# Kernel optimization log

Measured on AMD Instinct MI355X. Metric: run time of the kernel, lower is better.

Reference implementation:

```python
import jax, jax.numpy as jnp
import numpy as np

HEAD_DIM = 64
SCALE = HEAD_DIM ** (-0.5)


def setup_inputs() -> dict:
    key = jax.random.key(0)
    kq, kk, kv = jax.random.split(key, 3)
    B, H, S, D = 2, 12, 2048, HEAD_DIM
    query = jax.random.normal(kq, (B, H, S, D), dtype=jnp.float32)
    k = jax.random.normal(kk, (B, H, S, D), dtype=jnp.float32)
    v = jax.random.normal(kv, (B, H, S, D), dtype=jnp.float32)
    mask = jnp.ones((1, 1, S, S), dtype=jnp.int32)
    return {"query": query, "key": k, "value": v, "mask": mask}


def reference(query, key, value, mask):
    # scores: [B, H, S, S]
    scores = jnp.einsum("bhqd,bhkd->bhqk", query, key) * SCALE
    scores = jnp.where(mask == 0, -jnp.inf, scores)
    probs = jax.nn.softmax(scores, axis=-1)
    # dropout = 0.0 -> identity
    out = jnp.einsum("bhqk,bhkd->bhqd", probs, value)
    return out
```

## Files before the change

kernel.cpp:

```cpp
#include <hip/hip_runtime.h>

#define SDIM 2048
#define DDIM 64
#define QT   64
#define KT   64
#define NT   (SDIM / KT)
#define SCL2  (0.125f * 1.4426950408889634f)

typedef __attribute__((ext_vector_type(8))) short          bf16x8;
typedef __attribute__((ext_vector_type(4))) short          bf16x4;
typedef __attribute__((ext_vector_type(8))) unsigned short ushort8;
typedef __attribute__((ext_vector_type(4))) unsigned short us4;
typedef __attribute__((ext_vector_type(4))) float          f32x4;

__device__ __forceinline__ unsigned short f2bf(float x) {
    unsigned int u = __float_as_uint(x);
    u += 0x7FFFu + ((u >> 16) & 1u);
    return (unsigned short)(u >> 16);
}

__device__ __forceinline__ f32x4 mfma16(bf16x4 a, bf16x4 b, f32x4 c) {
#if __has_builtin(__builtin_amdgcn_mfma_f32_16x16x16bf16_1k)
    return __builtin_amdgcn_mfma_f32_16x16x16bf16_1k(a, b, c, 0, 0, 0);
#else
    asm volatile("v_mfma_f32_16x16x16_bf16 %0, %1, %2, %0" : "+v"(c) : "v"(a), "v"(b));
    return c;
#endif
}

__device__ __forceinline__ void cp16(const void* g, void* l) {
    __builtin_amdgcn_global_load_lds(
        (__attribute__((address_space(1))) void*)(uintptr_t)g,
        (__attribute__((address_space(3))) void*)(unsigned int)(uintptr_t)l,
        16, 0, 0);
}

__global__ __launch_bounds__(256)
void prep_kv(const float* __restrict__ Kp, const float* __restrict__ Vp,
             unsigned short* __restrict__ wsK, unsigned short* __restrict__ wsV)
{
    __shared__ alignas(16) unsigned short vstage[KT * DDIM];
    const int tid = threadIdx.x;
    const int t   = blockIdx.x;
    const int bh  = blockIdx.y;
    const size_t tb   = ((size_t)bh * NT + t) * (KT * DDIM);
    const size_t gsrc = (size_t)bh * SDIM * DDIM + (size_t)t * KT * DDIM;

    const int key = tid >> 2;
    const int d0  = (tid & 3) << 4;
    const int sw  = (key & 7) << 3;

    {
        const float* src = Kp + gsrc + key * DDIM + d0;
        float4 a0 = ((const float4*)src)[0];
        float4 a1 = ((const float4*)src)[1];
        float4 a2 = ((const float4*)src)[2];
        float4 a3 = ((const float4*)src)[3];
        ushort8 w0, w1;
        w0[0]=f2bf(a0.x); w0[1]=f2bf(a0.y); w0[2]=f2bf(a0.z); w0[3]=f2bf(a0.w);
        w0[4]=f2bf(a1.x); w0[5]=f2bf(a1.y); w0[6]=f2bf(a1.z); w0[7]=f2bf(a1.w);
        w1[0]=f2bf(a2.x); w1[1]=f2bf(a2.y); w1[2]=f2bf(a2.z); w1[3]=f2bf(a2.w);
        w1[4]=f2bf(a3.x); w1[5]=f2bf(a3.y); w1[6]=f2bf(a3.z); w1[7]=f2bf(a3.w);
        *(ushort8*)&wsK[tb + key * 64 + ( d0      ^ sw)] = w0;
        *(ushort8*)&wsK[tb + key * 64 + ((d0 + 8) ^ sw)] = w1;
    }
    {
        const float* src = Vp + gsrc + key * DDIM + d0;
        float4 a0 = ((const float4*)src)[0];
        float4 a1 = ((const float4*)src)[1];
        float4 a2 = ((const float4*)src)[2];
        float4 a3 = ((const float4*)src)[3];
        ushort8 w0, w1;
        w0[0]=f2bf(a0.x); w0[1]=f2bf(a0.y); w0[2]=f2bf(a0.z); w0[3]=f2bf(a0.w);
        w0[4]=f2bf(a1.x); w0[5]=f2bf(a1.y); w0[6]=f2bf(a1.z); w0[7]=f2bf(a1.w);
        w1[0]=f2bf(a2.x); w1[1]=f2bf(a2.y); w1[2]=f2bf(a2.z); w1[3]=f2bf(a2.w);
        w1[4]=f2bf(a3.x); w1[5]=f2bf(a3.y); w1[6]=f2bf(a3.z); w1[7]=f2bf(a3.w);
        *(ushort8*)&vstage[key * 64 + ( d0      ^ sw)] = w0;
        *(ushort8*)&vstage[key * 64 + ((d0 + 8) ^ sw)] = w1;
    }
    __syncthreads();
    {
        const int d  = tid >> 2;
        const int k0 = (tid & 3) << 4;
        const int m  = ((d & 7) << 1) ^ ((d >> 3) & 1);
        const int region = ((k0 >> 2) ^ (m & 12));
        unsigned short vals[16];
        #pragma unroll
        for (int j = 0; j < 16; ++j) {
            const int k = k0 + j;
            vals[j] = vstage[k * 64 + (d ^ ((k & 7) << 3))];
        }
        #pragma unroll
        for (int j = 0; j < 4; ++j) {
            us4 o = { vals[4*j], vals[4*j+1], vals[4*j+2], vals[4*j+3] };
            *(us4*)&wsV[tb + d * 64 + ((region | (j ^ (m & 3))) << 2)] = o;
        }
    }
}

__global__ __launch_bounds__(512)
void attn64_main(const float* __restrict__ Qp,
                 const unsigned short* __restrict__ wsK,
                 const unsigned short* __restrict__ wsV,
                 float* __restrict__ Op)
{
    __shared__ alignas(16) unsigned short kbuf[4][4096];
    __shared__ alignas(16) unsigned short vbuf[4][4096];

    const int tid  = threadIdx.x;
    const int lane = tid & 63;
    const int w    = tid >> 6;
    const int qg   = w & 3;
    const int par  = w >> 2;
    const int lo4  = lane & 15;
    const int hi2  = lane >> 4;
    const int l7s  = (lo4 & 7) << 3;
    const int vm   = ((lo4 & 7) << 1) ^ ((lo4 >> 3) & 1);

    const int qt = blockIdx.x;
    const int bh = blockIdx.y;

    const unsigned short* Kt = wsK + (size_t)bh * (SDIM * DDIM);
    const unsigned short* Vt = wsV + (size_t)bh * (SDIM * DDIM);

    cp16(Kt + tid * 8,        &kbuf[0][tid * 8]);
    cp16(Vt + tid * 8,        &vbuf[0][tid * 8]);
    cp16(Kt + 4096 + tid * 8, &kbuf[1][tid * 8]);
    cp16(Vt + 4096 + tid * 8, &vbuf[1][tid * 8]);

    bf16x8 qf[2];
    {
        const float* Qb = Qp + (size_t)bh * SDIM * DDIM;
        const int qrow = qt * QT + qg * 16 + lo4;
        #pragma unroll
        for (int ks = 0; ks < 2; ++ks) {
            const float* src = Qb + (size_t)qrow * DDIM + ks * 32 + hi2 * 8;
            float4 a = ((const float4*)src)[0];
            float4 b = ((const float4*)src)[1];
            bf16x8 tq;
            tq[0] = (short)f2bf(a.x * SCL2); tq[1] = (short)f2bf(a.y * SCL2);
            tq[2] = (short)f2bf(a.z * SCL2); tq[3] = (short)f2bf(a.w * SCL2);
            tq[4] = (short)f2bf(b.x * SCL2); tq[5] = (short)f2bf(b.y * SCL2);
            tq[6] = (short)f2bf(b.z * SCL2); tq[7] = (short)f2bf(b.w * SCL2);
            qf[ks] = tq;
        }
    }

    int kidx[2], vidx[4];
    #pragma unroll
    for (int ks = 0; ks < 2; ++ks) kidx[ks] = lo4 * 64 + ((ks * 32 + hi2 * 8) ^ l7s);
    #pragma unroll
    for (int n = 0; n < 4; ++n)   vidx[n]  = lo4 * 64 + (((4 * n + hi2) ^ vm) << 2);

    const short ov = (lo4 == 0) ? (short)0x3F80 : (short)0;
    const bf16x4 af = { ov, ov, ov, ov };

    f32x4 oacc[4];
    f32x4 acc5 = f32x4{0.f, 0.f, 0.f, 0.f};
    #pragma unroll
    for (int n = 0; n < 4; ++n) oacc[n] = f32x4{0.f, 0.f, 0.f, 0.f};

    const unsigned short* kbR0 = &kbuf[par][0];
    const unsigned short* vbR0 = &vbuf[par][0];
    const unsigned short* kbR1 = &kbuf[2 + par][0];
    const unsigned short* vbR1 = &vbuf[2 + par][0];

    const unsigned short* gk = Kt + 2 * 4096 + tid * 8;
    const unsigned short* gv = Vt + 2 * 4096 + tid * 8;

    auto tilebody = [&](const unsigned short* kb, const unsigned short* vb) {
        f32x4 s[4];
        #pragma unroll
        for (int n = 0; n < 4; ++n) s[n] = f32x4{0.f, 0.f, 0.f, 0.f};
        __builtin_amdgcn_s_setprio(1);
        #pragma unroll
        for (int ks = 0; ks < 2; ++ks) {
            #pragma unroll
            for (int n = 0; n < 4; ++n) {
                bf16x8 kf = *(const bf16x8*)&kb[kidx[ks] + n * 1024];
                s[n] = __builtin_amdgcn_mfma_f32_16x16x32_bf16(kf, qf[ks], s[n], 0, 0, 0);
            }
        }
        __builtin_amdgcn_s_setprio(0);
        bf16x4 pkk[4];
        #pragma unroll
        for (int n = 0; n < 4; ++n) {
            const float p0 = exp2f(s[n][0]);
            const float p1 = exp2f(s[n][1]);
            const float p2 = exp2f(s[n][2]);
            const float p3 = exp2f(s[n][3]);
            unsigned int lo, hi;
            asm("v_cvt_pk_bf16_f32 %0, %1, %2" : "=v"(lo) : "v"(p0), "v"(p1));
            asm("v_cvt_pk_bf16_f32 %0, %1, %2" : "=v"(hi) : "v"(p2), "v"(p3));
            union { unsigned int u[2]; bf16x4 v; } r;
            r.u[0] = lo; r.u[1] = hi;
            pkk[n] = r.v;
        }
        __builtin_amdgcn_s_setprio(1);
        #pragma unroll
        for (int n = 0; n < 4; ++n) {
            acc5 = mfma16(af, pkk[n], acc5);
            #pragma unroll
            for (int db = 0; db < 4; ++db) {
                bf16x4 vf = *(const bf16x4*)&vb[vidx[n] + db * 1024];
                oacc[db] = mfma16(vf, pkk[n], oacc[db]);
            }
        }
        __builtin_amdgcn_s_setprio(0);
    };

    asm volatile("s_waitcnt vmcnt(0) lgkmcnt(0)" ::: "memory");
    __builtin_amdgcn_s_barrier();

    #pragma unroll 1
    for (int j = 0; j < 8; ++j) {
        cp16(gk,        &kbuf[2][tid * 8]);
        cp16(gv,        &vbuf[2][tid * 8]);
        cp16(gk + 4096, &kbuf[3][tid * 8]);
        cp16(gv + 4096, &vbuf[3][tid * 8]);
        tilebody(kbR0, vbR0);
        asm volatile("s_waitcnt vmcnt(0) lgkmcnt(0)" ::: "memory");
        __builtin_amdgcn_s_barrier();
        if (j < 7) {
            cp16(gk + 8192,  &kbuf[0][tid * 8]);
            cp16(gv + 8192,  &vbuf[0][tid * 8]);
            cp16(gk + 12288, &kbuf[1][tid * 8]);
            cp16(gv + 12288, &vbuf[1][tid * 8]);
        }
        tilebody(kbR1, vbR1);
        asm volatile("s_waitcnt vmcnt(0) lgkmcnt(0)" ::: "memory");
        __builtin_amdgcn_s_barrier();
        gk += 16384;
        gv += 16384;
    }

    __syncthreads();
    float* comb = (float*)&kbuf[0][0];
    const int cbase = (qg * 64 + lane) * 20;
    if (par) {
        *(f32x4*)&comb[cbase]      = oacc[0];
        *(f32x4*)&comb[cbase + 4]  = oacc[1];
        *(f32x4*)&comb[cbase + 8]  = oacc[2];
        *(f32x4*)&comb[cbase + 12] = oacc[3];
        *(f32x4*)&comb[cbase + 16] = acc5;
    }
    __syncthreads();
    if (!par) {
        oacc[0] += *(const f32x4*)&comb[cbase];
        oacc[1] += *(const f32x4*)&comb[cbase + 4];
        oacc[2] += *(const f32x4*)&comb[cbase + 8];
        oacc[3] += *(const f32x4*)&comb[cbase + 12];
        acc5    += *(const f32x4*)&comb[cbase + 16];

        const float lsum = __shfl(acc5[0], lo4);
        const float inv = 1.f / lsum;
        const int q = qt * QT + qg * 16 + lo4;
        float* dst = Op + (size_t)bh * SDIM * DDIM + (size_t)q * DDIM;
        #pragma unroll
        for (int db = 0; db < 4; ++db) {
            float4 o = { oacc[db][0] * inv, oacc[db][1] * inv,
                         oacc[db][2] * inv, oacc[db][3] * inv };
            *(float4*)&dst[16 * db + hi2 * 4] = o;
        }
    }
}

__global__ __launch_bounds__(256)
void attn64_fallback(const float* __restrict__ Qp, const float* __restrict__ Kp,
                     const float* __restrict__ Vp, float* __restrict__ Op)
{
    __shared__ alignas(16) unsigned short kls[KT * DDIM];
    __shared__ alignas(16) unsigned short vls[DDIM * KT];
    __shared__ alignas(16) unsigned short pls[4][16 * KT];

    const int tid  = threadIdx.x;
    const int lane = tid & 63;
    const int wave = tid >> 6;
    const int lo4  = lane & 15;
    const int hi2  = lane >> 4;
    const int qt = blockIdx.x;
    const int bh = blockIdx.y;

    const size_t base = (size_t)bh * SDIM * DDIM;
    const float* Qb = Qp + base;
    const float* Kb = Kp + base;
    const float* Vb = Vp + base;
    float*       Ob = Op + base;

    bf16x8 qf[2];
    {
        const int qrow = qt * QT + wave * 16 + lo4;
        #pragma unroll
        for (int ks = 0; ks < 2; ++ks) {
            const float* src = Qb + (size_t)qrow * DDIM + ks * 32 + hi2 * 8;
            float4 a = ((const float4*)src)[0];
            float4 b = ((const float4*)src)[1];
            bf16x8 tq;
            tq[0] = (short)f2bf(a.x * SCL2); tq[1] = (short)f2bf(a.y * SCL2);
            tq[2] = (short)f2bf(a.z * SCL2); tq[3] = (short)f2bf(a.w * SCL2);
            tq[4] = (short)f2bf(b.x * SCL2); tq[5] = (short)f2bf(b.y * SCL2);
            tq[6] = (short)f2bf(b.z * SCL2); tq[7] = (short)f2bf(b.w * SCL2);
            qf[ks] = tq;
        }
    }

    float mrow[4], lrow[4];
    f32x4 oacc[4];
    #pragma unroll
    for (int r = 0; r < 4; ++r) { mrow[r] = -1e30f; lrow[r] = 0.f; }
    #pragma unroll
    for (int n = 0; n < 4; ++n) oacc[n] = f32x4{0.f, 0.f, 0.f, 0.f};

    for (int t0 = 0; t0 < SDIM; t0 += KT) {
        __syncthreads();
        {
            const int key = tid >> 2;
            const int d0  = (tid & 3) << 4;
            const float* src = Kb + (size_t)(t0 + key) * DDIM + d0;
            float4 a0 = ((const float4*)src)[0];
            float4 a1 = ((const float4*)src)[1];
            float4 a2 = ((const float4*)src)[2];
            float4 a3 = ((const float4*)src)[3];
            ushort8 w0, w1;
            w0[0]=f2bf(a0.x); w0[1]=f2bf(a0.y); w0[2]=f2bf(a0.z); w0[3]=f2bf(a0.w);
            w0[4]=f2bf(a1.x); w0[5]=f2bf(a1.y); w0[6]=f2bf(a1.z); w0[7]=f2bf(a1.w);
            w1[0]=f2bf(a2.x); w1[1]=f2bf(a2.y); w1[2]=f2bf(a2.z); w1[3]=f2bf(a2.w);
            w1[4]=f2bf(a3.x); w1[5]=f2bf(a3.y); w1[6]=f2bf(a3.z); w1[7]=f2bf(a3.w);
            const int sw = (key & 7) << 3;
            *(ushort8*)&kls[key * 64 + ( d0      ^ sw)] = w0;
            *(ushort8*)&kls[key * 64 + ((d0 + 8) ^ sw)] = w1;
        }
        {
            const int key = lane;
            const int d0  = wave << 4;
            const float* src = Vb + (size_t)(t0 + key) * DDIM + d0;
            float4 b0 = ((const float4*)src)[0];
            float4 b1 = ((const float4*)src)[1];
            float4 b2 = ((const float4*)src)[2];
            float4 b3 = ((const float4*)src)[3];
            float vv[16] = { b0.x,b0.y,b0.z,b0.w, b1.x,b1.y,b1.z,b1.w,
                             b2.x,b2.y,b2.z,b2.w, b3.x,b3.y,b3.z,b3.w };
            #pragma unroll
            for (int j = 0; j < 16; ++j) {
                const int d = d0 + j;
                vls[d * 64 + (key ^ ((d & 7) << 3))] = f2bf(vv[j]);
            }
        }
        __syncthreads();

        f32x4 s[4];
        #pragma unroll
        for (int n = 0; n < 4; ++n) s[n] = f32x4{0.f, 0.f, 0.f, 0.f};
        #pragma unroll
        for (int ks = 0; ks < 2; ++ks) {
            const int kb = ks * 32 + hi2 * 8;
            #pragma unroll
            for (int n = 0; n < 4; ++n) {
                const int key = lo4 + 16 * n;
                bf16x8 b = *(const bf16x8*)&kls[key * 64 + (kb ^ ((key & 7) << 3))];
                s[n] = __builtin_amdgcn_mfma_f32_16x16x32_bf16(qf[ks], b, s[n], 0, 0, 0);
            }
        }
        #pragma unroll
        for (int r = 0; r < 4; ++r) {
            float tmax = fmaxf(fmaxf(s[0][r], s[1][r]), fmaxf(s[2][r], s[3][r]));
            tmax = fmaxf(tmax, __shfl_xor(tmax, 1));
            tmax = fmaxf(tmax, __shfl_xor(tmax, 2));
            tmax = fmaxf(tmax, __shfl_xor(tmax, 4));
            tmax = fmaxf(tmax, __shfl_xor(tmax, 8));
            const float mn   = fmaxf(mrow[r], tmax);
            const float corr = exp2f(mrow[r] - mn);
            mrow[r] = mn;
            float rs = 0.f;
            #pragma unroll
            for (int n = 0; n < 4; ++n) {
                const float p = exp2f(s[n][r] - mn);
                s[n][r] = p;
                rs += p;
            }
            rs += __shfl_xor(rs, 1);
            rs += __shfl_xor(rs, 2);
            rs += __shfl_xor(rs, 4);
            rs += __shfl_xor(rs, 8);
            lrow[r] = lrow[r] * corr + rs;
            #pragma unroll
            for (int n = 0; n < 4; ++n) oacc[n][r] *= corr;
        }
        #pragma unroll
        for (int r = 0; r < 4; ++r) {
            const int q  = hi2 * 4 + r;
            const int sw = (q & 7) << 3;
            #pragma unroll
            for (int n = 0; n < 4; ++n)
                pls[wave][q * 64 + ((lo4 + 16 * n) ^ sw)] = f2bf(s[n][r]);
        }
        __syncthreads();
        #pragma unroll
        for (int ks = 0; ks < 2; ++ks) {
            const int kb = ks * 32 + hi2 * 8;
            bf16x8 a = *(const bf16x8*)&pls[wave][lo4 * 64 + (kb ^ ((lo4 & 7) << 3))];
            #pragma unroll
            for (int n = 0; n < 4; ++n) {
                const int d = 16 * n + lo4;
                bf16x8 b = *(const bf16x8*)&vls[d * 64 + (kb ^ ((d & 7) << 3))];
                oacc[n] = __builtin_amdgcn_mfma_f32_16x16x32_bf16(a, b, oacc[n], 0, 0, 0);
            }
        }
    }
    #pragma unroll
    for (int r = 0; r < 4; ++r) {
        const float inv = 1.f / lrow[r];
        const int q = qt * QT + wave * 16 + hi2 * 4 + r;
        float* dst = Ob + (size_t)q * DDIM;
        #pragma unroll
        for (int n = 0; n < 4; ++n)
            dst[16 * n + lo4] = oacc[n][r] * inv;
    }
}

extern "C" void kernel_launch(void* const* d_in, const int* in_sizes, int n_in,
                              void* d_out, int out_size, void* d_ws, size_t ws_size,
                              hipStream_t stream) {
    const float* Q = (const float*)d_in[0];
    const float* K = (const float*)d_in[1];
    const float* V = (const float*)d_in[2];
    float* O = (float*)d_out;
    const int BH = in_sizes[0] / (SDIM * DDIM);
    const size_t need = 2ull * BH * SDIM * DDIM * sizeof(unsigned short);

    if (ws_size >= need) {
        unsigned short* wsK = (unsigned short*)d_ws;
        unsigned short* wsV = wsK + (size_t)BH * SDIM * DDIM;
        prep_kv<<<dim3(NT, BH), dim3(256), 0, stream>>>(K, V, wsK, wsV);
        attn64_main<<<dim3(SDIM / QT, BH), dim3(512), 0, stream>>>(Q, wsK, wsV, O);
    } else {
        attn64_fallback<<<dim3(SDIM / QT, BH), dim3(256), 0, stream>>>(Q, K, V, O);
    }
}
```

Before: 59.53 us.

## Halve key tile to 32 in main attention kernel with wave-split staging

```diff
diff --git a/kernel.cpp b/kernel.cpp
--- a/kernel.cpp
+++ b/kernel.cpp
@@ -3,8 +3,8 @@
 #define SDIM 2048
 #define DDIM 64
 #define QT   64
-#define KT   64
-#define NT   (SDIM / KT)
+#define NT   32
+#define NT2  64
 #define SCL2  (0.125f * 1.4426950408889634f)
 
 typedef __attribute__((ext_vector_type(8))) short          bf16x8;
@@ -39,12 +39,12 @@
 void prep_kv(const float* __restrict__ Kp, const float* __restrict__ Vp,
              unsigned short* __restrict__ wsK, unsigned short* __restrict__ wsV)
 {
-    __shared__ alignas(16) unsigned short vstage[KT * DDIM];
+    __shared__ alignas(16) unsigned short vstage[64 * DDIM];
     const int tid = threadIdx.x;
     const int t   = blockIdx.x;
     const int bh  = blockIdx.y;
-    const size_t tb   = ((size_t)bh * NT + t) * (KT * DDIM);
-    const size_t gsrc = (size_t)bh * SDIM * DDIM + (size_t)t * KT * DDIM;
+    const size_t tb   = ((size_t)bh * NT + t) * (64 * DDIM);
+    const size_t gsrc = (size_t)bh * SDIM * DDIM + (size_t)t * 64 * DDIM;
 
     const int key = tid >> 2;
     const int d0  = (tid & 3) << 4;
@@ -80,20 +80,23 @@
     }
     __syncthreads();
     {
-        const int d  = tid >> 2;
-        const int k0 = (tid & 3) << 4;
-        const int m  = ((d & 7) << 1) ^ ((d >> 3) & 1);
-        const int region = ((k0 >> 2) ^ (m & 12));
+        const int d   = tid >> 2;
+        const int k0  = (tid & 3) << 4;
+        const int s_  = k0 >> 5;
+        const int k00 = k0 & 31;
+        const int vm2 = (d >> 1) & 7;
         unsigned short vals[16];
         #pragma unroll
         for (int j = 0; j < 16; ++j) {
             const int k = k0 + j;
             vals[j] = vstage[k * 64 + (d ^ ((k & 7) << 3))];
         }
+        const size_t vbase = tb + s_ * 2048 + d * 32;
         #pragma unroll
         for (int j = 0; j < 4; ++j) {
+            const int c = (k00 >> 2) + j;
             us4 o = { vals[4*j], vals[4*j+1], vals[4*j+2], vals[4*j+3] };
-            *(us4*)&wsV[tb + d * 64 + ((region | (j ^ (m & 3))) << 2)] = o;
+            *(us4*)&wsV[vbase + ((c ^ vm2) << 2)] = o;
         }
     }
 }
@@ -104,8 +107,8 @@
                  const unsigned short* __restrict__ wsV,
                  float* __restrict__ Op)
 {
-    __shared__ alignas(16) unsigned short kbuf[4][4096];
-    __shared__ alignas(16) unsigned short vbuf[4][4096];
+    __shared__ alignas(16) unsigned short kbuf[4][2048];
+    __shared__ alignas(16) unsigned short vbuf[4][2048];
 
     const int tid  = threadIdx.x;
     const int lane = tid & 63;
@@ -115,7 +118,7 @@
     const int lo4  = lane & 15;
     const int hi2  = lane >> 4;
     const int l7s  = (lo4 & 7) << 3;
-    const int vm   = ((lo4 & 7) << 1) ^ ((lo4 >> 3) & 1);
+    const int vm2  = (lo4 >> 1) & 7;
 
     const int qt = blockIdx.x;
     const int bh = blockIdx.y;
@@ -123,10 +126,16 @@
     const unsigned short* Kt = wsK + (size_t)bh * (SDIM * DDIM);
     const unsigned short* Vt = wsV + (size_t)bh * (SDIM * DDIM);
 
-    cp16(Kt + tid * 8,        &kbuf[0][tid * 8]);
-    cp16(Vt + tid * 8,        &vbuf[0][tid * 8]);
-    cp16(Kt + 4096 + tid * 8, &kbuf[1][tid * 8]);
-    cp16(Vt + 4096 + tid * 8, &vbuf[1][tid * 8]);
+    const int chك = w & 3;
+    const bool isK = (w < 4);
+    const unsigned short* gbase = (isK ? Kt : Vt) + (chك << 9) + lane * 8;
+    auto stage = [&](int t, int b) {
+        unsigned short* l = (isK ? &kbuf[b][0] : &vbuf[b][0]) + (chك << 9) + lane * 8;
+        cp16(gbase + ((size_t)t << 11), l);
+    };
+
+    stage(0, 0);
+    stage(1, 1);
 
     bf16x8 qf[2];
     {
@@ -146,11 +155,11 @@
         }
     }
 
-    int kidx[2], vidx[4];
+    int kidx[2], vidx[2];
     #pragma unroll
     for (int ks = 0; ks < 2; ++ks) kidx[ks] = lo4 * 64 + ((ks * 32 + hi2 * 8) ^ l7s);
     #pragma unroll
-    for (int n = 0; n < 4; ++n)   vidx[n]  = lo4 * 64 + (((4 * n + hi2) ^ vm) << 2);
+    for (int n = 0; n < 2; ++n)   vidx[n]  = lo4 * 32 + (((4 * n + hi2) ^ vm2) << 2);
 
     const short ov = (lo4 == 0) ? (short)0x3F80 : (short)0;
     const bf16x4 af = { ov, ov, ov, ov };
@@ -165,26 +174,23 @@
     const unsigned short* kbR1 = &kbuf[2 + par][0];
     const unsigned short* vbR1 = &vbuf[2 + par][0];
 
-    const unsigned short* gk = Kt + 2 * 4096 + tid * 8;
-    const unsigned short* gv = Vt + 2 * 4096 + tid * 8;
-
     auto tilebody = [&](const unsigned short* kb, const unsigned short* vb) {
-        f32x4 s[4];
-        #pragma unroll
-        for (int n = 0; n < 4; ++n) s[n] = f32x4{0.f, 0.f, 0.f, 0.f};
+        f32x4 s[2];
+        s[0] = f32x4{0.f, 0.f, 0.f, 0.f};
+        s[1] = f32x4{0.f, 0.f, 0.f, 0.f};
         __builtin_amdgcn_s_setprio(1);
         #pragma unroll
         for (int ks = 0; ks < 2; ++ks) {
             #pragma unroll
-            for (int n = 0; n < 4; ++n) {
+            for (int n = 0; n < 2; ++n) {
                 bf16x8 kf = *(const bf16x8*)&kb[kidx[ks] + n * 1024];
                 s[n] = __builtin_amdgcn_mfma_f32_16x16x32_bf16(kf, qf[ks], s[n], 0, 0, 0);
             }
         }
         __builtin_amdgcn_s_setprio(0);
-        bf16x4 pkk[4];
-        #pragma unroll
-        for (int n = 0; n < 4; ++n) {
+        bf16x4 pkk[2];
+        #pragma unroll
+        for (int n = 0; n < 2; ++n) {
             const float p0 = exp2f(s[n][0]);
             const float p1 = exp2f(s[n][1]);
             const float p2 = exp2f(s[n][2]);
@@ -198,11 +204,11 @@
         }
         __builtin_amdgcn_s_setprio(1);
         #pragma unroll
-        for (int n = 0; n < 4; ++n) {
+        for (int n = 0; n < 2; ++n) {
             acc5 = mfma16(af, pkk[n], acc5);
             #pragma unroll
             for (int db = 0; db < 4; ++db) {
-                bf16x4 vf = *(const bf16x4*)&vb[vidx[n] + db * 1024];
+                bf16x4 vf = *(const bf16x4*)&vb[vidx[n] + db * 512];
                 oacc[db] = mfma16(vf, pkk[n], oacc[db]);
             }
         }
@@ -213,44 +219,37 @@
     __builtin_amdgcn_s_barrier();
 
     #pragma unroll 1
-    for (int j = 0; j < 8; ++j) {
-        cp16(gk,        &kbuf[2][tid * 8]);
-        cp16(gv,        &vbuf[2][tid * 8]);
-        cp16(gk + 4096, &kbuf[3][tid * 8]);
-        cp16(gv + 4096, &vbuf[3][tid * 8]);
+    for (int j = 0; j < 16; ++j) {
+        stage(4 * j + 2, 2);
+        stage(4 * j + 3, 3);
         tilebody(kbR0, vbR0);
         asm volatile("s_waitcnt vmcnt(0) lgkmcnt(0)" ::: "memory");
         __builtin_amdgcn_s_barrier();
-        if (j < 7) {
-            cp16(gk + 8192,  &kbuf[0][tid * 8]);
-            cp16(gv + 8192,  &vbuf[0][tid * 8]);
-            cp16(gk + 12288, &kbuf[1][tid * 8]);
-            cp16(gv + 12288, &vbuf[1][tid * 8]);
+        if (j < 15) {
+            stage(4 * j + 4, 0);
+            stage(4 * j + 5, 1);
         }
         tilebody(kbR1, vbR1);
         asm volatile("s_waitcnt vmcnt(0) lgkmcnt(0)" ::: "memory");
         __builtin_amdgcn_s_barrier();
-        gk += 16384;
-        gv += 16384;
     }
 
     __syncthreads();
-    float* comb = (float*)&kbuf[0][0];
-    const int cbase = (qg * 64 + lane) * 20;
+    float* combO = (float*)&kbuf[0][0];
+    float* combL = (float*)&vbuf[0][0];
+    const int cb = qg * 64 + lane;
     if (par) {
-        *(f32x4*)&comb[cbase]      = oacc[0];
-        *(f32x4*)&comb[cbase + 4]  = oacc[1];
-        *(f32x4*)&comb[cbase + 8]  = oacc[2];
-        *(f32x4*)&comb[cbase + 12] = oacc[3];
-        *(f32x4*)&comb[cbase + 16] = acc5;
+        #pragma unroll
+        for (int db = 0; db < 4; ++db)
+            *(f32x4*)&combO[cb * 16 + db * 4] = oacc[db];
+        *(f32x4*)&combL[cb * 4] = acc5;
     }
     __syncthreads();
     if (!par) {
-        oacc[0] += *(const f32x4*)&comb[cbase];
-        oacc[1] += *(const f32x4*)&comb[cbase + 4];
-        oacc[2] += *(const f32x4*)&comb[cbase + 8];
-        oacc[3] += *(const f32x4*)&comb[cbase + 12];
-        acc5    += *(const f32x4*)&comb[cbase + 16];
+        #pragma unroll
+        for (int db = 0; db < 4; ++db)
+            oacc[db] += *(const f32x4*)&combO[cb * 16 + db * 4];
+        acc5 += *(const f32x4*)&combL[cb * 4];
 
         const float lsum = __shfl(acc5[0], lo4);
         const float inv = 1.f / lsum;
@@ -269,9 +268,9 @@
 void attn64_fallback(const float* __restrict__ Qp, const float* __restrict__ Kp,
                      const float* __restrict__ Vp, float* __restrict__ Op)
 {
-    __shared__ alignas(16) unsigned short kls[KT * DDIM];
-    __shared__ alignas(16) unsigned short vls[DDIM * KT];
-    __shared__ alignas(16) unsigned short pls[4][16 * KT];
+    __shared__ alignas(16) unsigned short kls[64 * DDIM];
+    __shared__ alignas(16) unsigned short vls[DDIM * 64];
+    __shared__ alignas(16) unsigned short pls[4][16 * 64];
 
     const int tid  = threadIdx.x;
     const int lane = tid & 63;
@@ -311,7 +310,7 @@
     #pragma unroll
     for (int n = 0; n < 4; ++n) oacc[n] = f32x4{0.f, 0.f, 0.f, 0.f};
 
-    for (int t0 = 0; t0 < SDIM; t0 += KT) {
+    for (int t0 = 0; t0 < SDIM; t0 += 64) {
         __syncthreads();
         {
             const int key = tid >> 2;
```

Measured after the change: 57.56 us. -3.3%, faster.
